# Kernel optimization log

Hardware: AMD Instinct MI355X
Metric: run time of the kernel (lower is better)

## Reference

```python
import jax, jax.numpy as jnp
import numpy as np

B, T, C = 4, 2048, 768
N_HEADS = 16
HEAD_DIM = C // N_HEADS  # 48
ROPE_BASE = 10000.0


def setup_inputs() -> dict:
    key = jax.random.key(0)
    ks = jax.random.split(key, 6)
    s = 0.02
    return {
        "hidden_states": jax.random.normal(ks[0], (B, T, C), dtype=jnp.float32),
        "attention_mask": jnp.ones((B, T), dtype=jnp.float32),
        "Wq": jax.random.normal(ks[1], (C, C), dtype=jnp.float32) * s,
        "bq": jnp.zeros((C,), dtype=jnp.float32),
        "Wk": jax.random.normal(ks[2], (C, C), dtype=jnp.float32) * s,
        "bk": jnp.zeros((C,), dtype=jnp.float32),
        "Wv": jax.random.normal(ks[3], (C, C), dtype=jnp.float32) * s,
        "bv": jnp.zeros((C,), dtype=jnp.float32),
        "Wo": jax.random.normal(ks[4], (C, C), dtype=jnp.float32) * s,
        "bo": jnp.zeros((C,), dtype=jnp.float32),
    }


def _rotate_half(x):
    x1, x2 = jnp.split(x, 2, axis=-1)
    return jnp.concatenate([-x2, x1], axis=-1)


def reference(hidden_states, attention_mask, Wq, bq, Wk, bk, Wv, bv, Wo, bo):
    b, t, c = hidden_states.shape
    h, d = N_HEADS, c // N_HEADS

    def split_heads(x):  # [b,t,c] -> [b,h,t,d]
        return x.reshape(b, t, h, d).transpose(0, 2, 1, 3)

    q = split_heads(hidden_states @ Wq.T + bq)
    k = split_heads(hidden_states @ Wk.T + bk)
    v = split_heads(hidden_states @ Wv.T + bv)

    # rotary embedding: cos/sin [t, d]
    pos = jnp.arange(t, dtype=jnp.float32)
    inv_freq = 1.0 / (ROPE_BASE ** (jnp.arange(0, d, 2, dtype=jnp.float32) / d))
    freqs = pos[:, None] * inv_freq[None, :]          # [t, d/2]
    emb = jnp.concatenate([freqs, freqs], axis=-1)    # [t, d]
    cos, sin = jnp.cos(emb), jnp.sin(emb)
    q = q * cos + _rotate_half(q) * sin
    k = k * cos + _rotate_half(k) * sin

    scores = jnp.einsum('bhqd,bhkd->bhqk', q, k) / jnp.sqrt(jnp.asarray(d, q.dtype))
    # additive padding mask: (1 - mask) * -10000, broadcast [b,1,1,t]
    scores = scores + (1.0 - attention_mask)[:, None, None, :] * -10000.0
    # causal mask with -inf
    causal = jnp.tril(jnp.ones((t, t), dtype=bool))
    scores = jnp.where(causal[None, None], scores, -jnp.inf)

    probs = jax.nn.softmax(scores, axis=-1)
    ctx = jnp.einsum('bhqk,bhkd->bhqd', probs, v)
    ctx = ctx.transpose(0, 2, 1, 3).reshape(b, t, c)
    return ctx @ Wo.T + bo
```

## Files before the change

kernel.cpp:

```cpp
#include <hip/hip_runtime.h>
#include <hip/hip_bf16.h>
#include <math.h>

#define BB 4
#define TT 2048
#define CC 768
#define NHD 16
#define HD 48
#define NQT2 16

typedef __hip_bfloat16 bf16;
typedef __attribute__((ext_vector_type(8))) short short8;
typedef __attribute__((ext_vector_type(4))) float floatx4;

__device__ __forceinline__ unsigned short f2bf(float x) {
    bf16 h = __float2bfloat16(x);
    return *(unsigned short*)&h;
}
__device__ __forceinline__ float bfu2f(unsigned short u) {
    return __uint_as_float(((unsigned)u) << 16);
}

__device__ __forceinline__ void gl_lds16(const void* g, void* s) {
    __builtin_amdgcn_global_load_lds((const __attribute__((address_space(1))) void*)g,
                                     (__attribute__((address_space(3))) void*)s, 16, 0, 0);
}

__device__ __forceinline__ unsigned int pk_bf2(float a, float b) {
    unsigned int ua = __float_as_uint(a) + 0x8000u;
    unsigned int ub = __float_as_uint(b) + 0x8000u;
    return __builtin_amdgcn_perm(ub, ua, 0x07060302);
}

#define HOT_BARRIER() asm volatile("s_waitcnt lgkmcnt(0)\n\ts_barrier" ::: "memory")

__global__ __launch_bounds__(256) void cast_hs(const float* __restrict__ src,
                                               unsigned short* __restrict__ dst) {
    int i = (blockIdx.x * 256 + threadIdx.x) * 4;
    float4 v = *(const float4*)(src + i);
    ushort4 p;
    p.x = f2bf(v.x); p.y = f2bf(v.y); p.z = f2bf(v.z); p.w = f2bf(v.w);
    *(ushort4*)(dst + i) = p;
}

__global__ __launch_bounds__(256) void cast_w4(const float* __restrict__ s0, const float* __restrict__ s1,
                                               const float* __restrict__ s2, const float* __restrict__ s3,
                                               unsigned short* __restrict__ d0, unsigned short* __restrict__ d1,
                                               unsigned short* __restrict__ d2, unsigned short* __restrict__ d3) {
    const float* s; unsigned short* d;
    switch (blockIdx.y) {
        case 0: s = s0; d = d0; break;
        case 1: s = s1; d = d1; break;
        case 2: s = s2; d = d2; break;
        default: s = s3; d = d3; break;
    }
    int i = (blockIdx.x * 256 + threadIdx.x) * 4;
    float4 v = *(const float4*)(s + i);
    ushort4 p;
    p.x = f2bf(v.x); p.y = f2bf(v.y); p.z = f2bf(v.z); p.w = f2bf(v.w);
    *(ushort4*)(d + i) = p;
}

__global__ __launch_bounds__(256) void rope_table(float2* __restrict__ tab) {
    int idx = blockIdx.x * 256 + threadIdx.x;
    int t = idx / 24, p = idx % 24;
    float inv_freq = powf(10000.0f, -((float)(2 * p) / (float)HD));
    float ang = (float)t * inv_freq;
    float sn, cs;
    sincosf(ang, &sn, &cs);
    tab[idx] = make_float2(cs, sn);
}

template <int MODE>
__global__ __launch_bounds__(256) void gemm_mfma(const unsigned short* __restrict__ A,
                                                 const unsigned short* __restrict__ Bw,
                                                 const float* __restrict__ b0p,
                                                 const float* __restrict__ b1p,
                                                 const float* __restrict__ b2p,
                                                 void* __restrict__ out0,
                                                 void* __restrict__ out1,
                                                 void* __restrict__ out2) {
    __shared__ __align__(16) unsigned short As[128][64];
    __shared__ __align__(16) unsigned short Bs[128][64];
    const int tid = threadIdx.x;
    const int w = tid >> 6, lane = tid & 63;
    const int quad = lane >> 4, ln = lane & 15;
    const int wr = w >> 1, wc = w & 1;

    const int NXB = (MODE == 1) ? 18 : 6;
    const int bx = blockIdx.x;
    const int xcd = bx & 7, slot = bx >> 3;
    const int n0 = (slot % NXB) * 128;
    const int m0 = ((slot / NXB) * 8 + xcd) * 128;

    const int srow = lane >> 3;
    const int ssw = ((lane & 7) ^ srow) * 8;
    const unsigned short* agp[4];
    const unsigned short* bgp[4];
    void* asl[4];
    void* bsl[4];
#pragma unroll
    for (int i = 0; i < 4; ++i) {
        const int R = i * 32 + w * 8;
        agp[i] = A + (size_t)(m0 + R + srow) * CC + ssw;
        bgp[i] = Bw + (size_t)(n0 + R + srow) * CC + ssw;
        asl[i] = &As[R][0];
        bsl[i] = &Bs[R][0];
    }

    floatx4 acc[4][4];
#pragma unroll
    for (int mi = 0; mi < 4; ++mi)
#pragma unroll
        for (int ni = 0; ni < 4; ++ni) acc[mi][ni] = (floatx4){0.f, 0.f, 0.f, 0.f};

    const int ps0 = (quad ^ (ln & 7)) * 8;

    for (int k0 = 0; k0 < CC; k0 += 64) {
        __syncthreads();
#pragma unroll
        for (int i = 0; i < 4; ++i) {
            gl_lds16(agp[i] + k0, asl[i]);
            gl_lds16(bgp[i] + k0, bsl[i]);
        }
        __syncthreads();
#pragma unroll
        for (int kh = 0; kh < 2; ++kh) {
            const int ps = ps0 ^ (kh * 32);
            short8 af[4], bfr[4];
#pragma unroll
            for (int mi = 0; mi < 4; ++mi)
                af[mi] = *(const short8*)&As[wr * 64 + mi * 16 + ln][ps];
#pragma unroll
            for (int ni = 0; ni < 4; ++ni)
                bfr[ni] = *(const short8*)&Bs[wc * 64 + ni * 16 + ln][ps];
#pragma unroll
            for (int mi = 0; mi < 4; ++mi)
#pragma unroll
                for (int ni = 0; ni < 4; ++ni)
                    acc[mi][ni] = __builtin_amdgcn_mfma_f32_16x16x32_bf16(af[mi], bfr[ni], acc[mi][ni], 0, 0, 0);
        }
    }

    if (MODE == 0) {
        float* outf = (float*)out0;
        float bv[4];
#pragma unroll
        for (int ni = 0; ni < 4; ++ni) bv[ni] = b0p[n0 + wc * 64 + ni * 16 + ln];
#pragma unroll
        for (int mi = 0; mi < 4; ++mi)
#pragma unroll
            for (int r = 0; r < 4; ++r) {
                size_t row = m0 + wr * 64 + mi * 16 + quad * 4 + r;
#pragma unroll
                for (int ni = 0; ni < 4; ++ni)
                    outf[row * CC + n0 + wc * 64 + ni * 16 + ln] = acc[mi][ni][r] + bv[ni];
            }
    } else {
        const int seg = n0 / CC;
        const int nl0 = n0 - seg * CC;
        const float* bp = (seg == 0) ? b0p : (seg == 1) ? b1p : b2p;
        float bv[4];
#pragma unroll
        for (int ni = 0; ni < 4; ++ni) bv[ni] = bp[nl0 + wc * 64 + ni * 16 + ln];

        if (seg < 2) {
            unsigned short* outb = (unsigned short*)(seg == 0 ? out0 : out1);
#pragma unroll
            for (int mi = 0; mi < 4; ++mi)
#pragma unroll
                for (int r = 0; r < 4; ++r) {
                    size_t row = m0 + wr * 64 + mi * 16 + quad * 4 + r;
#pragma unroll
                    for (int ni = 0; ni < 4; ++ni)
                        outb[row * CC + nl0 + wc * 64 + ni * 16 + ln] = f2bf(acc[mi][ni][r] + bv[ni]);
                }
        } else {
            unsigned short* outb = (unsigned short*)out2;
            const int b = m0 >> 11;
#pragma unroll
            for (int ni = 0; ni < 4; ++ni) {
                int col = nl0 + wc * 64 + ni * 16 + ln;
                int h = col / HD, d = col % HD;
                size_t base = (size_t)((b * NHD + h) * HD + d) * TT;
#pragma unroll
                for (int mi = 0; mi < 4; ++mi) {
                    int t = (m0 & 2047) + wr * 64 + mi * 16 + quad * 4;
                    ushort4 pk;
                    pk.x = f2bf(acc[mi][ni][0] + bv[ni]);
                    pk.y = f2bf(acc[mi][ni][1] + bv[ni]);
                    pk.z = f2bf(acc[mi][ni][2] + bv[ni]);
                    pk.w = f2bf(acc[mi][ni][3] + bv[ni]);
                    *(ushort4*)(outb + base + t) = pk;
                }
            }
        }
    }
}

__global__ __launch_bounds__(256) void rope_bf(unsigned short* __restrict__ q,
                                               unsigned short* __restrict__ k,
                                               const float2* __restrict__ tab) {
    int idx = blockIdx.x * blockDim.x + threadIdx.x;
    const int HALF = HD / 2;
    int p8 = idx % 3;
    int rest = idx / 3;
    int h = rest % NHD;
    int n = rest / NHD;
    int t = n & (TT - 1);
    const float QSC = 0.14433756729740643f * 1.4426950408889634f;
    size_t base = (size_t)n * CC + h * HD + p8 * 8;
    const float2* tp = tab + t * HALF + p8 * 8;

    short8 q1 = *(const short8*)(q + base);
    short8 q2 = *(const short8*)(q + base + HALF);
    short8 k1 = *(const short8*)(k + base);
    short8 k2 = *(const short8*)(k + base + HALF);
    short8 r1, r2, s1, s2;
#pragma unroll
    for (int jj = 0; jj < 8; ++jj) {
        float2 cssn = tp[jj];
        float cs = cssn.x, sn = cssn.y;
        float a = bfu2f((unsigned short)q1[jj]), bb = bfu2f((unsigned short)q2[jj]);
        r1[jj] = (short)f2bf((a * cs - bb * sn) * QSC);
        r2[jj] = (short)f2bf((bb * cs + a * sn) * QSC);
        float c2 = bfu2f((unsigned short)k1[jj]), d2 = bfu2f((unsigned short)k2[jj]);
        s1[jj] = (short)f2bf(c2 * cs - d2 * sn);
        s2[jj] = (short)f2bf(d2 * cs + c2 * sn);
    }
    *(short8*)(q + base) = r1;
    *(short8*)(q + base + HALF) = r2;
    *(short8*)(k + base) = s1;
    *(short8*)(k + base + HALF) = s2;
}

__global__ __launch_bounds__(256, 2) void attn_kernel(const unsigned short* __restrict__ qb,
                                                      const unsigned short* __restrict__ kb,
                                                      const unsigned short* __restrict__ vt,
                                                      const float* __restrict__ amask,
                                                      unsigned short* __restrict__ ctx) {
    const int bx = blockIdx.x;
    const int xcd = bx & 7;
    const int rem = bx >> 3;
    const int pair = rem & 7;
    const int j = ((rem >> 3) << 3) | xcd;
    const int b = j >> 4, h = j & 15;
    const int tid = threadIdx.x;
    const int w = tid >> 6, lane = tid & 63;
    const int g = lane >> 4, ln = lane & 15;
    const int sw = ln & 7;

    __shared__ __align__(16) unsigned short Ks[64][64];
    __shared__ __align__(16) unsigned short Vs[48][64];
    __shared__ __align__(16) unsigned short Pw[4][32][64];
    __shared__ __align__(16) float l_s[4][32];

    const short8 z8 = {0, 0, 0, 0, 0, 0, 0, 0};
    const short8 ones8 = {0x3F80, 0x3F80, 0x3F80, 0x3F80, 0x3F80, 0x3F80, 0x3F80, 0x3F80};

    if (tid < 128) {
        int rr = tid >> 1, half = tid & 1;
        *(short8*)&Ks[rr][((6 + half) ^ (rr & 7)) * 8] = z8;
    }

    const int ck1 = tid + 256;
    const int rK0 = tid / 6, sK0 = tid % 6;
    const int rK1 = ck1 / 6, sK1 = ck1 % 6;
    const int swK0 = (sK0 ^ (rK0 & 7)) * 8;
    const int swK1 = (sK1 ^ (rK1 & 7)) * 8;
    const int rV0 = tid >> 3, sV0 = tid & 7;
    const int rV1 = rV0 + 32;
    const int swV0 = (sV0 ^ (rV0 & 7)) * 8;
    const int swV1 = (sV0 ^ (rV1 & 7)) * 8;

    const unsigned short* kbase0 = kb + (size_t)(b * TT + rK0) * CC + h * HD + sK0 * 8;
    const unsigned short* kbase1 = kb + (size_t)(b * TT + rK1) * CC + h * HD + sK1 * 8;
    const unsigned short* vbase0 = vt + ((size_t)((b * NHD + h) * HD) + rV0) * TT + sV0 * 8;
    const unsigned short* vbase1 = vbase0 + (size_t)32 * TT;
    const float* mbase = amask + b * TT + (tid & 63);
    const float MBS = -10000.0f * 1.4426950408889634f;
    const int mcol = (6 ^ (lane & 7)) * 8;
    const short8 vone = (ln == 0) ? ones8 : z8;

    for (int rep = 0; rep < 2; ++rep) {
        const int qt = rep ? (NQT2 - 1 - pair) : pair;
        const int q0 = qt * 128;
        const int last = 2 * qt + 1;

        const unsigned short* qrA = qb + (size_t)(b * TT + q0 + w * 16 + ln) * CC + h * HD;
        const unsigned short* qrB = qrA + (size_t)64 * CC;
        short8 aq0a = *(const short8*)(qrA + g * 8);
        short8 aq0b = *(const short8*)(qrB + g * 8);
        short8 aq1a, aq1b;
        if (g < 2) {
            aq1a = *(const short8*)(qrA + 32 + g * 8);
            aq1b = *(const short8*)(qrB + 32 + g * 8);
        } else {
            aq1a = z8; aq1b = z8;
            if (g == 2) { aq1a[0] = (short)0x3F80; aq1b[0] = (short)0x3F80; }
        }

        const unsigned short* kp0 = kbase0;
        const unsigned short* kp1 = kbase1;
        const unsigned short* vp0 = vbase0;
        const unsigned short* vp1 = vbase1;
        const float* mp = mbase;

        short8 kr0, kr1, vr0, vr1;
        float mr = 1.0f;
        kr0 = *(const short8*)kp0;
        vr0 = *(const short8*)vp0;
        if (tid < 128) { kr1 = *(const short8*)kp1; vr1 = *(const short8*)vp1; }
        if (tid < 64) mr = *mp;

        const int qlA = q0 + w * 16 + ln;
        const int qlB = qlA + 64;
        floatx4 oa0 = {0.f, 0.f, 0.f, 0.f}, oa1 = oa0, oa2 = oa0, oa3 = oa0;
        floatx4 ob0 = oa0, ob1 = oa0, ob2 = oa0, ob3 = oa0;

        for (int kt = 0; kt <= last; ++kt) {
            HOT_BARRIER();
            *(short8*)&Ks[rK0][swK0] = kr0;
            *(short8*)&Vs[rV0][swV0] = vr0;
            if (tid < 128) {
                *(short8*)&Ks[rK1][swK1] = kr1;
                *(short8*)&Vs[rV1][swV1] = vr1;
            }
            if (tid < 64) Ks[lane][mcol] = f2bf((1.0f - mr) * MBS);
            HOT_BARRIER();

            if (kt < last) {
                kp0 += (size_t)64 * CC; kr0 = *(const short8*)kp0;
                vp0 += 64;              vr0 = *(const short8*)vp0;
                if (tid < 128) {
                    kp1 += (size_t)64 * CC; kr1 = *(const short8*)kp1;
                    vp1 += 64;              vr1 = *(const short8*)vp1;
                }
                if (tid < 64) { mp += 64; mr = *mp; }
            }

            const int k0 = kt * 64;
            const bool a_act = (kt <= 2 * qt);
            const bool diagA = (kt == 2 * qt);
            const bool diagB = (kt == last);

            floatx4 sa[4], sb[4];
#pragma unroll
            for (int c = 0; c < 4; ++c) {
                short8 kf0 = *(const short8*)&Ks[c * 16 + ln][(g ^ sw) * 8];
                short8 kf1 = *(const short8*)&Ks[c * 16 + ln][((4 + g) ^ sw) * 8];
                floatx4 z = {0.f, 0.f, 0.f, 0.f};
                if (a_act) {
                    floatx4 za = __builtin_amdgcn_mfma_f32_16x16x32_bf16(kf0, aq0a, z, 0, 0, 0);
                    sa[c] = __builtin_amdgcn_mfma_f32_16x16x32_bf16(kf1, aq1a, za, 0, 0, 0);
                }
                floatx4 zb = __builtin_amdgcn_mfma_f32_16x16x32_bf16(kf0, aq0b, z, 0, 0, 0);
                sb[c] = __builtin_amdgcn_mfma_f32_16x16x32_bf16(kf1, aq1b, zb, 0, 0, 0);
            }

            if (a_act) {
#pragma unroll
                for (int c = 0; c < 4; ++c) {
                    float pv[4];
#pragma unroll
                    for (int r = 0; r < 4; ++r) {
                        float e = __builtin_amdgcn_exp2f(sa[c][r]);
                        if (diagA && (k0 + c * 16 + g * 4 + r > qlA)) e = 0.f;
                        pv[r] = e;
                    }
                    uint2 pk;
                    pk.x = pk_bf2(pv[0], pv[1]);
                    pk.y = pk_bf2(pv[2], pv[3]);
                    *(uint2*)&Pw[w][ln][((2 * c + (g >> 1)) ^ sw) * 8 + (g & 1) * 4] = pk;
                }
            }
#pragma unroll
            for (int c = 0; c < 4; ++c) {
                float pv[4];
#pragma unroll
                for (int r = 0; r < 4; ++r) {
                    float e = __builtin_amdgcn_exp2f(sb[c][r]);
                    if (diagB && (k0 + c * 16 + g * 4 + r > qlB)) e = 0.f;
                    pv[r] = e;
                }
                uint2 pk;
                pk.x = pk_bf2(pv[0], pv[1]);
                pk.y = pk_bf2(pv[2], pv[3]);
                *(uint2*)&Pw[w][16 + ln][((2 * c + (g >> 1)) ^ sw) * 8 + (g & 1) * 4] = pk;
            }

            short8 pa0a, pa1a;
            if (a_act) {
                pa0a = *(const short8*)&Pw[w][ln][(g ^ sw) * 8];
                pa1a = *(const short8*)&Pw[w][ln][((4 + g) ^ sw) * 8];
            }
            short8 pa0b = *(const short8*)&Pw[w][16 + ln][(g ^ sw) * 8];
            short8 pa1b = *(const short8*)&Pw[w][16 + ln][((4 + g) ^ sw) * 8];

#pragma unroll
            for (int n = 0; n < 3; ++n) {
                short8 vb0 = *(const short8*)&Vs[n * 16 + ln][(g ^ sw) * 8];
                short8 vb1 = *(const short8*)&Vs[n * 16 + ln][((4 + g) ^ sw) * 8];
                if (a_act) {
                    floatx4 acc = (n == 0) ? oa0 : (n == 1) ? oa1 : oa2;
                    acc = __builtin_amdgcn_mfma_f32_16x16x32_bf16(pa0a, vb0, acc, 0, 0, 0);
                    acc = __builtin_amdgcn_mfma_f32_16x16x32_bf16(pa1a, vb1, acc, 0, 0, 0);
                    if (n == 0) oa0 = acc; else if (n == 1) oa1 = acc; else oa2 = acc;
                }
                floatx4 accb = (n == 0) ? ob0 : (n == 1) ? ob1 : ob2;
                accb = __builtin_amdgcn_mfma_f32_16x16x32_bf16(pa0b, vb0, accb, 0, 0, 0);
                accb = __builtin_amdgcn_mfma_f32_16x16x32_bf16(pa1b, vb1, accb, 0, 0, 0);
                if (n == 0) ob0 = accb; else if (n == 1) ob1 = accb; else ob2 = accb;
            }
            if (a_act) {
                oa3 = __builtin_amdgcn_mfma_f32_16x16x32_bf16(pa0a, vone, oa3, 0, 0, 0);
                oa3 = __builtin_amdgcn_mfma_f32_16x16x32_bf16(pa1a, vone, oa3, 0, 0, 0);
            }
            ob3 = __builtin_amdgcn_mfma_f32_16x16x32_bf16(pa0b, vone, ob3, 0, 0, 0);
            ob3 = __builtin_amdgcn_mfma_f32_16x16x32_bf16(pa1b, vone, ob3, 0, 0, 0);
        }

        if (ln == 0) {
            *(floatx4*)&l_s[w][g * 4] = oa3;
            *(floatx4*)&l_s[w][16 + g * 4] = ob3;
        }
        floatx4 l4a = *(const floatx4*)&l_s[w][g * 4];
        floatx4 l4b = *(const floatx4*)&l_s[w][16 + g * 4];
#pragma unroll
        for (int r = 0; r < 4; ++r) {
            float invA = 1.0f / l4a[r];
            int t = q0 + w * 16 + g * 4 + r;
            unsigned short* dst = ctx + (size_t)(b * TT + t) * CC + h * HD;
            dst[ln] = f2bf(oa0[r] * invA);
            dst[16 + ln] = f2bf(oa1[r] * invA);
            dst[32 + ln] = f2bf(oa2[r] * invA);
            float invB = 1.0f / l4b[r];
            unsigned short* dstB = dst + (size_t)64 * CC;
            dstB[ln] = f2bf(ob0[r] * invB);
            dstB[16 + ln] = f2bf(ob1[r] * invB);
            dstB[32 + ln] = f2bf(ob2[r] * invB);
        }
    }
}

extern "C" void kernel_launch(void* const* d_in, const int* in_sizes, int n_in,
                              void* d_out, int out_size, void* d_ws, size_t ws_size,
                              hipStream_t stream) {
    const float* hs = (const float*)d_in[0];
    const float* amask = (const float*)d_in[1];
    const float* Wq = (const float*)d_in[2];
    const float* bq = (const float*)d_in[3];
    const float* Wk = (const float*)d_in[4];
    const float* bk = (const float*)d_in[5];
    const float* Wv = (const float*)d_in[6];
    const float* bv = (const float*)d_in[7];
    const float* Wo = (const float*)d_in[8];
    const float* bo = (const float*)d_in[9];

    const size_t NELEM = (size_t)BB * TT * CC;
    const size_t WELEM = (size_t)CC * CC;
    unsigned short* hb  = (unsigned short*)d_ws;
    unsigned short* qbuf = hb + NELEM;
    unsigned short* kbuf = qbuf + NELEM;
    unsigned short* vtb = kbuf + NELEM;
    unsigned short* ctxb = vtb + NELEM;
    unsigned short* wqb = ctxb + NELEM;
    unsigned short* wkb = wqb + WELEM;
    unsigned short* wvb = wkb + WELEM;
    unsigned short* wob = wvb + WELEM;
    float2* ropetab = (float2*)(wob + WELEM);

    cast_hs<<<NELEM / 1024, 256, 0, stream>>>(hs, hb);
    dim3 wgrid(WELEM / 1024, 4);
    cast_w4<<<wgrid, 256, 0, stream>>>(Wq, Wk, Wv, Wo, wqb, wkb, wvb, wob);
    rope_table<<<(TT * (HD / 2)) / 256, 256, 0, stream>>>(ropetab);

    gemm_mfma<1><<<18 * 64, 256, 0, stream>>>(hb, wqb, bq, bk, bv, qbuf, kbuf, vtb);

    int rope_total = BB * TT * NHD * 3;
    rope_bf<<<rope_total / 256, 256, 0, stream>>>(qbuf, kbuf, ropetab);

    attn_kernel<<<512, 256, 0, stream>>>(qbuf, kbuf, vtb, amask, ctxb);

    gemm_mfma<0><<<6 * 64, 256, 0, stream>>>(ctxb, wob, bo, nullptr, nullptr,
                                             (float*)d_out, nullptr, nullptr);
}
```

Measured before the change: 221.2 us.

## Shrink attention query tile to 64 rows with 128-thread blocks and more workgroups

The attention kernel now uses 128-thread workgroups (2 waves), each handling 64 query rows per tile instead of 128, and launches 1024 blocks instead of 512. Block-to-(b,h,tile) mapping is reworked so that each wave owns 32 contiguous rows, and causal masking happens only on the single diagonal key tile. This removes the half-active a_act branches. Probability packing switches to the hardware v_cvt_pk_bf16_f32 instruction. The aim is better load balance and occupancy, at the cost of loading K/V tiles twice as often per query row.

```diff
diff --git a/kernel.cpp b/kernel.cpp
--- a/kernel.cpp
+++ b/kernel.cpp
@@ -7,7 +7,7 @@
 #define CC 768
 #define NHD 16
 #define HD 48
-#define NQT2 16
+#define NQT 32
 
 typedef __hip_bfloat16 bf16;
 typedef __attribute__((ext_vector_type(8))) short short8;
@@ -30,6 +30,12 @@
     unsigned int ua = __float_as_uint(a) + 0x8000u;
     unsigned int ub = __float_as_uint(b) + 0x8000u;
     return __builtin_amdgcn_perm(ub, ua, 0x07060302);
+}
+
+__device__ __forceinline__ unsigned int cvtpk(float lo, float hi) {
+    unsigned int r;
+    asm("v_cvt_pk_bf16_f32 %0, %1, %2" : "=v"(r) : "v"(lo), "v"(hi));
+    return r;
 }
 
 #define HOT_BARRIER() asm volatile("s_waitcnt lgkmcnt(0)\n\ts_barrier" ::: "memory")
@@ -234,16 +240,17 @@
     *(short8*)(k + base + HALF) = s2;
 }
 
-__global__ __launch_bounds__(256, 2) void attn_kernel(const unsigned short* __restrict__ qb,
+__global__ __launch_bounds__(128, 2) void attn_kernel(const unsigned short* __restrict__ qb,
                                                       const unsigned short* __restrict__ kb,
                                                       const unsigned short* __restrict__ vt,
                                                       const float* __restrict__ amask,
                                                       unsigned short* __restrict__ ctx) {
     const int bx = blockIdx.x;
     const int xcd = bx & 7;
-    const int rem = bx >> 3;
-    const int pair = rem & 7;
-    const int j = ((rem >> 3) << 3) | xcd;
+    const int s = bx >> 3;
+    const int bh_l = s & 7;
+    const int pairidx = s >> 3;
+    const int j = (bh_l << 3) | xcd;
     const int b = j >> 4, h = j & 15;
     const int tid = threadIdx.x;
     const int w = tid >> 6, lane = tid & 63;
@@ -252,43 +259,48 @@
 
     __shared__ __align__(16) unsigned short Ks[64][64];
     __shared__ __align__(16) unsigned short Vs[48][64];
-    __shared__ __align__(16) unsigned short Pw[4][32][64];
-    __shared__ __align__(16) float l_s[4][32];
+    __shared__ __align__(16) unsigned short Pw[2][32][64];
+    __shared__ __align__(16) float l_s[2][32];
 
     const short8 z8 = {0, 0, 0, 0, 0, 0, 0, 0};
     const short8 ones8 = {0x3F80, 0x3F80, 0x3F80, 0x3F80, 0x3F80, 0x3F80, 0x3F80, 0x3F80};
 
-    if (tid < 128) {
-        int rr = tid >> 1, half = tid & 1;
+    {
+        int rr = tid & 63, half = tid >> 6;
         *(short8*)&Ks[rr][((6 + half) ^ (rr & 7)) * 8] = z8;
     }
 
-    const int ck1 = tid + 256;
-    const int rK0 = tid / 6, sK0 = tid % 6;
-    const int rK1 = ck1 / 6, sK1 = ck1 % 6;
-    const int swK0 = (sK0 ^ (rK0 & 7)) * 8;
-    const int swK1 = (sK1 ^ (rK1 & 7)) * 8;
-    const int rV0 = tid >> 3, sV0 = tid & 7;
-    const int rV1 = rV0 + 32;
-    const int swV0 = (sV0 ^ (rV0 & 7)) * 8;
-    const int swV1 = (sV0 ^ (rV1 & 7)) * 8;
-
+    const int u0 = tid, u1 = tid + 128, u2 = tid + 256;
+    const int rK0 = u0 / 6, sK0 = u0 % 6;
+    const int rK1 = u1 / 6, sK1 = u1 % 6;
+    const int rK2 = u2 / 6, sK2 = u2 % 6;
+    const int rV0 = u0 >> 3, sV0 = u0 & 7;
+    const int rV1 = u1 >> 3, sV1 = u1 & 7;
+    const int rV2 = u2 >> 3, sV2 = u2 & 7;
+    unsigned short* dK0 = &Ks[rK0][(sK0 ^ (rK0 & 7)) * 8];
+    unsigned short* dK1 = &Ks[rK1][(sK1 ^ (rK1 & 7)) * 8];
+    unsigned short* dK2 = &Ks[rK2][(sK2 ^ (rK2 & 7)) * 8];
+    unsigned short* dV0 = &Vs[rV0][(sV0 ^ (rV0 & 7)) * 8];
+    unsigned short* dV1 = &Vs[rV1][(sV1 ^ (rV1 & 7)) * 8];
+    unsigned short* dV2 = &Vs[rV2][(sV2 ^ (rV2 & 7)) * 8];
     const unsigned short* kbase0 = kb + (size_t)(b * TT + rK0) * CC + h * HD + sK0 * 8;
     const unsigned short* kbase1 = kb + (size_t)(b * TT + rK1) * CC + h * HD + sK1 * 8;
+    const unsigned short* kbase2 = kb + (size_t)(b * TT + rK2) * CC + h * HD + sK2 * 8;
     const unsigned short* vbase0 = vt + ((size_t)((b * NHD + h) * HD) + rV0) * TT + sV0 * 8;
-    const unsigned short* vbase1 = vbase0 + (size_t)32 * TT;
+    const unsigned short* vbase1 = vt + ((size_t)((b * NHD + h) * HD) + rV1) * TT + sV1 * 8;
+    const unsigned short* vbase2 = vt + ((size_t)((b * NHD + h) * HD) + rV2) * TT + sV2 * 8;
     const float* mbase = amask + b * TT + (tid & 63);
     const float MBS = -10000.0f * 1.4426950408889634f;
-    const int mcol = (6 ^ (lane & 7)) * 8;
+    const int mcol = (6 ^ (tid & 7)) * 8;
     const short8 vone = (ln == 0) ? ones8 : z8;
+    const int rowA = w * 32 + ln;
 
     for (int rep = 0; rep < 2; ++rep) {
-        const int qt = rep ? (NQT2 - 1 - pair) : pair;
-        const int q0 = qt * 128;
-        const int last = 2 * qt + 1;
-
-        const unsigned short* qrA = qb + (size_t)(b * TT + q0 + w * 16 + ln) * CC + h * HD;
-        const unsigned short* qrB = qrA + (size_t)64 * CC;
+        const int qt = rep ? (NQT - 1 - pairidx) : pairidx;
+        const int q0 = qt * 64;
+
+        const unsigned short* qrA = qb + (size_t)(b * TT + q0 + w * 32 + ln) * CC + h * HD;
+        const unsigned short* qrB = qrA + (size_t)16 * CC;
         short8 aq0a = *(const short8*)(qrA + g * 8);
         short8 aq0b = *(const short8*)(qrB + g * 8);
         short8 aq1a, aq1b;
@@ -302,98 +314,81 @@
 
         const unsigned short* kp0 = kbase0;
         const unsigned short* kp1 = kbase1;
+        const unsigned short* kp2 = kbase2;
         const unsigned short* vp0 = vbase0;
         const unsigned short* vp1 = vbase1;
+        const unsigned short* vp2 = vbase2;
         const float* mp = mbase;
 
-        short8 kr0, kr1, vr0, vr1;
-        float mr = 1.0f;
-        kr0 = *(const short8*)kp0;
-        vr0 = *(const short8*)vp0;
-        if (tid < 128) { kr1 = *(const short8*)kp1; vr1 = *(const short8*)vp1; }
-        if (tid < 64) mr = *mp;
-
-        const int qlA = q0 + w * 16 + ln;
-        const int qlB = qlA + 64;
+        short8 kr0 = *(const short8*)kp0;
+        short8 kr1 = *(const short8*)kp1;
+        short8 kr2 = *(const short8*)kp2;
+        short8 vr0 = *(const short8*)vp0;
+        short8 vr1 = *(const short8*)vp1;
+        short8 vr2 = *(const short8*)vp2;
+        float mr = (tid < 64) ? *mp : 1.0f;
+
         floatx4 oa0 = {0.f, 0.f, 0.f, 0.f}, oa1 = oa0, oa2 = oa0, oa3 = oa0;
         floatx4 ob0 = oa0, ob1 = oa0, ob2 = oa0, ob3 = oa0;
 
-        for (int kt = 0; kt <= last; ++kt) {
+        for (int kt = 0; kt <= qt; ++kt) {
             HOT_BARRIER();
-            *(short8*)&Ks[rK0][swK0] = kr0;
-            *(short8*)&Vs[rV0][swV0] = vr0;
-            if (tid < 128) {
-                *(short8*)&Ks[rK1][swK1] = kr1;
-                *(short8*)&Vs[rV1][swV1] = vr1;
-            }
-            if (tid < 64) Ks[lane][mcol] = f2bf((1.0f - mr) * MBS);
+            *(short8*)dK0 = kr0; *(short8*)dK1 = kr1; *(short8*)dK2 = kr2;
+            *(short8*)dV0 = vr0; *(short8*)dV1 = vr1; *(short8*)dV2 = vr2;
+            if (tid < 64) Ks[tid][mcol] = f2bf((1.0f - mr) * MBS);
             HOT_BARRIER();
 
-            if (kt < last) {
+            if (kt < qt) {
                 kp0 += (size_t)64 * CC; kr0 = *(const short8*)kp0;
-                vp0 += 64;              vr0 = *(const short8*)vp0;
-                if (tid < 128) {
-                    kp1 += (size_t)64 * CC; kr1 = *(const short8*)kp1;
-                    vp1 += 64;              vr1 = *(const short8*)vp1;
-                }
+                kp1 += (size_t)64 * CC; kr1 = *(const short8*)kp1;
+                kp2 += (size_t)64 * CC; kr2 = *(const short8*)kp2;
+                vp0 += 64; vr0 = *(const short8*)vp0;
+                vp1 += 64; vr1 = *(const short8*)vp1;
+                vp2 += 64; vr2 = *(const short8*)vp2;
                 if (tid < 64) { mp += 64; mr = *mp; }
             }
 
-            const int k0 = kt * 64;
-            const bool a_act = (kt <= 2 * qt);
-            const bool diagA = (kt == 2 * qt);
-            const bool diagB = (kt == last);
-
-            floatx4 sa[4], sb[4];
+            const bool masked = (kt == qt);
+
+            floatx4 sa_[4], sb_[4];
 #pragma unroll
             for (int c = 0; c < 4; ++c) {
                 short8 kf0 = *(const short8*)&Ks[c * 16 + ln][(g ^ sw) * 8];
                 short8 kf1 = *(const short8*)&Ks[c * 16 + ln][((4 + g) ^ sw) * 8];
                 floatx4 z = {0.f, 0.f, 0.f, 0.f};
-                if (a_act) {
-                    floatx4 za = __builtin_amdgcn_mfma_f32_16x16x32_bf16(kf0, aq0a, z, 0, 0, 0);
-                    sa[c] = __builtin_amdgcn_mfma_f32_16x16x32_bf16(kf1, aq1a, za, 0, 0, 0);
+                floatx4 za = __builtin_amdgcn_mfma_f32_16x16x32_bf16(kf0, aq0a, z, 0, 0, 0);
+                sa_[c] = __builtin_amdgcn_mfma_f32_16x16x32_bf16(kf1, aq1a, za, 0, 0, 0);
+                floatx4 zb = __builtin_amdgcn_mfma_f32_16x16x32_bf16(kf0, aq0b, z, 0, 0, 0);
+                sb_[c] = __builtin_amdgcn_mfma_f32_16x16x32_bf16(kf1, aq1b, zb, 0, 0, 0);
+            }
+
+#pragma unroll
+            for (int c = 0; c < 4; ++c) {
+                float pva[4], pvb[4];
+#pragma unroll
+                for (int r = 0; r < 4; ++r) {
+                    pva[r] = __builtin_amdgcn_exp2f(sa_[c][r]);
+                    pvb[r] = __builtin_amdgcn_exp2f(sb_[c][r]);
                 }
-                floatx4 zb = __builtin_amdgcn_mfma_f32_16x16x32_bf16(kf0, aq0b, z, 0, 0, 0);
-                sb[c] = __builtin_amdgcn_mfma_f32_16x16x32_bf16(kf1, aq1b, zb, 0, 0, 0);
-            }
-
-            if (a_act) {
-#pragma unroll
-                for (int c = 0; c < 4; ++c) {
-                    float pv[4];
+                if (masked) {
 #pragma unroll
                     for (int r = 0; r < 4; ++r) {
-                        float e = __builtin_amdgcn_exp2f(sa[c][r]);
-                        if (diagA && (k0 + c * 16 + g * 4 + r > qlA)) e = 0.f;
-                        pv[r] = e;
+                        int kcol = c * 16 + g * 4 + r;
+                        if (kcol > rowA) pva[r] = 0.f;
+                        if (kcol > rowA + 16) pvb[r] = 0.f;
                     }
-                    uint2 pk;
-                    pk.x = pk_bf2(pv[0], pv[1]);
-                    pk.y = pk_bf2(pv[2], pv[3]);
-                    *(uint2*)&Pw[w][ln][((2 * c + (g >> 1)) ^ sw) * 8 + (g & 1) * 4] = pk;
                 }
-            }
-#pragma unroll
-            for (int c = 0; c < 4; ++c) {
-                float pv[4];
-#pragma unroll
-                for (int r = 0; r < 4; ++r) {
-                    float e = __builtin_amdgcn_exp2f(sb[c][r]);
-                    if (diagB && (k0 + c * 16 + g * 4 + r > qlB)) e = 0.f;
-                    pv[r] = e;
-                }
-                uint2 pk;
-                pk.x = pk_bf2(pv[0], pv[1]);
-                pk.y = pk_bf2(pv[2], pv[3]);
-                *(uint2*)&Pw[w][16 + ln][((2 * c + (g >> 1)) ^ sw) * 8 + (g & 1) * 4] = pk;
-            }
-
-            short8 pa0a, pa1a;
-            if (a_act) {
-                pa0a = *(const short8*)&Pw[w][ln][(g ^ sw) * 8];
-                pa1a = *(const short8*)&Pw[w][ln][((4 + g) ^ sw) * 8];
-            }
+                uint2 pka, pkb;
+                pka.x = cvtpk(pva[0], pva[1]);
+                pka.y = cvtpk(pva[2], pva[3]);
+                pkb.x = cvtpk(pvb[0], pvb[1]);
+                pkb.y = cvtpk(pvb[2], pvb[3]);
+                *(uint2*)&Pw[w][ln][((2 * c + (g >> 1)) ^ sw) * 8 + (g & 1) * 4] = pka;
+                *(uint2*)&Pw[w][16 + ln][((2 * c + (g >> 1)) ^ sw) * 8 + (g & 1) * 4] = pkb;
+            }
+
+            short8 pa0a = *(const short8*)&Pw[w][ln][(g ^ sw) * 8];
+            short8 pa1a = *(const short8*)&Pw[w][ln][((4 + g) ^ sw) * 8];
             short8 pa0b = *(const short8*)&Pw[w][16 + ln][(g ^ sw) * 8];
             short8 pa1b = *(const short8*)&Pw[w][16 + ln][((4 + g) ^ sw) * 8];
 
@@ -401,21 +396,17 @@
             for (int n = 0; n < 3; ++n) {
                 short8 vb0 = *(const short8*)&Vs[n * 16 + ln][(g ^ sw) * 8];
                 short8 vb1 = *(const short8*)&Vs[n * 16 + ln][((4 + g) ^ sw) * 8];
-                if (a_act) {
-                    floatx4 acc = (n == 0) ? oa0 : (n == 1) ? oa1 : oa2;
-                    acc = __builtin_amdgcn_mfma_f32_16x16x32_bf16(pa0a, vb0, acc, 0, 0, 0);
-                    acc = __builtin_amdgcn_mfma_f32_16x16x32_bf16(pa1a, vb1, acc, 0, 0, 0);
-                    if (n == 0) oa0 = acc; else if (n == 1) oa1 = acc; else oa2 = acc;
-                }
+                floatx4 acc = (n == 0) ? oa0 : (n == 1) ? oa1 : oa2;
+                acc = __builtin_amdgcn_mfma_f32_16x16x32_bf16(pa0a, vb0, acc, 0, 0, 0);
+                acc = __builtin_amdgcn_mfma_f32_16x16x32_bf16(pa1a, vb1, acc, 0, 0, 0);
+                if (n == 0) oa0 = acc; else if (n == 1) oa1 = acc; else oa2 = acc;
                 floatx4 accb = (n == 0) ? ob0 : (n == 1) ? ob1 : ob2;
                 accb = __builtin_amdgcn_mfma_f32_16x16x32_bf16(pa0b, vb0, accb, 0, 0, 0);
                 accb = __builtin_amdgcn_mfma_f32_16x16x32_bf16(pa1b, vb1, accb, 0, 0, 0);
                 if (n == 0) ob0 = accb; else if (n == 1) ob1 = accb; else ob2 = accb;
             }
-            if (a_act) {
-                oa3 = __builtin_amdgcn_mfma_f32_16x16x32_bf16(pa0a, vone, oa3, 0, 0, 0);
-                oa3 = __builtin_amdgcn_mfma_f32_16x16x32_bf16(pa1a, vone, oa3, 0, 0, 0);
-            }
+            oa3 = __builtin_amdgcn_mfma_f32_16x16x32_bf16(pa0a, vone, oa3, 0, 0, 0);
+            oa3 = __builtin_amdgcn_mfma_f32_16x16x32_bf16(pa1a, vone, oa3, 0, 0, 0);
             ob3 = __builtin_amdgcn_mfma_f32_16x16x32_bf16(pa0b, vone, ob3, 0, 0, 0);
             ob3 = __builtin_amdgcn_mfma_f32_16x16x32_bf16(pa1b, vone, ob3, 0, 0, 0);
         }
@@ -429,13 +420,13 @@
 #pragma unroll
         for (int r = 0; r < 4; ++r) {
             float invA = 1.0f / l4a[r];
-            int t = q0 + w * 16 + g * 4 + r;
+            int t = q0 + w * 32 + g * 4 + r;
             unsigned short* dst = ctx + (size_t)(b * TT + t) * CC + h * HD;
             dst[ln] = f2bf(oa0[r] * invA);
             dst[16 + ln] = f2bf(oa1[r] * invA);
             dst[32 + ln] = f2bf(oa2[r] * invA);
             float invB = 1.0f / l4b[r];
-            unsigned short* dstB = dst + (size_t)64 * CC;
+            unsigned short* dstB = dst + (size_t)16 * CC;
             dstB[ln] = f2bf(ob0[r] * invB);
             dstB[16 + ln] = f2bf(ob1[r] * invB);
             dstB[32 + ln] = f2bf(ob2[r] * invB);
@@ -480,7 +471,7 @@
     int rope_total = BB * TT * NHD * 3;
     rope_bf<<<rope_total / 256, 256, 0, stream>>>(qbuf, kbuf, ropetab);
 
-    attn_kernel<<<512, 256, 0, stream>>>(qbuf, kbuf, vtb, amask, ctxb);
+    attn_kernel<<<1024, 128, 0, stream>>>(qbuf, kbuf, vtb, amask, ctxb);
 
     gemm_mfma<0><<<6 * 64, 256, 0, stream>>>(ctxb, wob, bo, nullptr, nullptr,
                                              (float*)d_out, nullptr, nullptr);
```

Result: slower. 226.3 us (+2.3%).
